# Optimization experiments

Measured on AMD Instinct MI355X. Metric: run time of the kernel, lower is better.

## Reference

```python
import jax, jax.numpy as jnp
import numpy as np

B, T, D, H = 4, 2048, 1024, 16
DK = D // H

def setup_inputs() -> dict:
    key = jax.random.key(0)
    k1, k2, k3 = jax.random.split(key, 3)
    s = 1.0 / np.sqrt(D)
    return {
        "x": jax.random.normal(k1, (B, T, D), dtype=jnp.float32),
        "W_qkv": jax.random.normal(k2, (D, 3 * D), dtype=jnp.float32) * s,
        "b_qkv": jnp.zeros((3 * D,), dtype=jnp.float32),
        "W_out": jax.random.normal(k3, (D, D), dtype=jnp.float32) * s,
        "b_out": jnp.zeros((D,), dtype=jnp.float32),
    }

def reference(x, W_qkv, b_qkv, W_out, b_out):
    Bx, Tx, C = x.shape
    qkv = x @ W_qkv + b_qkv                       # [B,T,3D]
    q, k, v = jnp.split(qkv, 3, axis=-1)
    # [B,T,D] -> [B,H,T,dk]
    def heads(t):
        return t.reshape(Bx, Tx, H, DK).transpose(0, 2, 1, 3)
    q, k, v = heads(q), heads(k), heads(v)
    scores = jnp.einsum('bhqd,bhkd->bhqk', q, k) / jnp.sqrt(jnp.float32(DK))
    causal = jnp.tril(jnp.ones((Tx, Tx), dtype=bool))  # [T,T]
    scores = jnp.where(causal[None, None], scores, -jnp.inf)
    attn = jax.nn.softmax(scores, axis=-1)        # dropout p=0 (eval)
    out = jnp.einsum('bhqk,bhkd->bhqd', attn, v)  # [B,H,T,dk]
    out = out.transpose(0, 2, 1, 3).reshape(Bx, Tx, C)
    return out @ W_out + b_out
```

## Files before the change

kernel.cpp:

```cpp
#include <hip/hip_runtime.h>
#include <hip/hip_bf16.h>
#include <stdint.h>

#define T_SEQ 2048
#define DMODEL 1024
#define NH 16
#define DKH 64
#define M_TOK 8192
#define N_QKV 3072
#define K_DIM 1024

#define ATTN_SC (0.125f * 1.44269504f)

typedef __attribute__((ext_vector_type(8))) short short8;
typedef __attribute__((ext_vector_type(4))) short short4v;
typedef __attribute__((ext_vector_type(4))) float float4v;
typedef __attribute__((ext_vector_type(2))) unsigned int uint2v;

__device__ inline short bf16_bits(float f) {
  __hip_bfloat16 h = __float2bfloat16(f);
  short s;
  __builtin_memcpy(&s, &h, 2);
  return s;
}

__device__ inline short4v pack4_bf16_fast(float a, float b, float c, float d) {
  unsigned ua = __builtin_bit_cast(unsigned, a) + 0x8000u;
  unsigned ub = __builtin_bit_cast(unsigned, b) + 0x8000u;
  unsigned uc = __builtin_bit_cast(unsigned, c) + 0x8000u;
  unsigned ud = __builtin_bit_cast(unsigned, d) + 0x8000u;
  uint2v uu = {(ua >> 16) | (ub & 0xFFFF0000u),
               (uc >> 16) | (ud & 0xFFFF0000u)};
  return __builtin_bit_cast(short4v, uu);
}

__device__ inline void async_load16(const void* g, void* l) {
  __builtin_amdgcn_global_load_lds(
      (const __attribute__((address_space(1))) unsigned int*)g,
      (__attribute__((address_space(3))) unsigned int*)l,
      16, 0, 0);
}


__global__ __launch_bounds__(256) void cvt_kernel(const float* __restrict__ in,
                                                  short* __restrict__ out, int n) {
  int idx = (blockIdx.x * 256 + threadIdx.x) * 4;
  if (idx < n) {
    float4v v = *(const float4v*)(in + idx);
    short4v o;
    o[0] = bf16_bits(v[0]); o[1] = bf16_bits(v[1]);
    o[2] = bf16_bits(v[2]); o[3] = bf16_bits(v[3]);
    *(short4v*)(out + idx) = o;
  }
}

__global__ __launch_bounds__(256) void transpose_cvt(const float* __restrict__ in,
                                                     short* __restrict__ out,
                                                     int K, int N) {
  __shared__ float tile[32][33];
  int n0 = blockIdx.x * 32, k0 = blockIdx.y * 32;
  int tx = threadIdx.x, ty = threadIdx.y;
  #pragma unroll
  for (int r = ty; r < 32; r += 8)
    tile[r][tx] = in[(size_t)(k0 + r) * N + n0 + tx];
  __syncthreads();
  #pragma unroll
  for (int r = ty; r < 32; r += 8)
    out[(size_t)(n0 + r) * K + k0 + tx] = bf16_bits(tile[tx][r]);
}


template <int MODE>
__global__ __launch_bounds__(256) void gemm_bt(
    const short* __restrict__ A, const short* __restrict__ Bt,
    const float* __restrict__ bias,
    short* __restrict__ Qb, short* __restrict__ Kf, short* __restrict__ Vf,
    float* __restrict__ Cout, int M, int N, int K) {
  __shared__ __align__(16) short As[128 * 32];
  __shared__ __align__(16) short Bs[128 * 32];
  const int tid = threadIdx.x;
  const int lane = tid & 63;
  const int wave = tid >> 6;
  const int m0 = blockIdx.y * 128;
  const int n0 = blockIdx.x * 128;
  const int wm = (wave >> 1) * 64;
  const int wn = (wave & 1) * 64;
  const int quad = lane >> 4;
  const int l16 = lane & 15;

  float4v acc[4][4] = {};

  const int r0 = tid >> 2,        o0 = (tid & 3) * 8;
  const int r1 = (tid + 256) >> 2, o1 = ((tid + 256) & 3) * 8;
  short* ldsA0 = As + (size_t)(wave * 64) * 8;
  short* ldsA1 = As + (size_t)(256 + wave * 64) * 8;
  short* ldsB0 = Bs + (size_t)(wave * 64) * 8;
  short* ldsB1 = Bs + (size_t)(256 + wave * 64) * 8;

  for (int kt = 0; kt < K; kt += 32) {
    async_load16(A  + (size_t)(m0 + r0) * K + kt + o0, ldsA0);
    async_load16(A  + (size_t)(m0 + r1) * K + kt + o1, ldsA1);
    async_load16(Bt + (size_t)(n0 + r0) * K + kt + o0, ldsB0);
    async_load16(Bt + (size_t)(n0 + r1) * K + kt + o1, ldsB1);
    __builtin_amdgcn_s_waitcnt(0);
    __syncthreads();

    short8 af[4], bfr[4];
    #pragma unroll
    for (int t = 0; t < 4; ++t)
      af[t] = *(const short8*)(As + (size_t)(wm + t * 16 + l16) * 32 + quad * 8);
    #pragma unroll
    for (int t = 0; t < 4; ++t)
      bfr[t] = *(const short8*)(Bs + (size_t)(wn + t * 16 + l16) * 32 + quad * 8);
    #pragma unroll
    for (int i = 0; i < 4; ++i)
      #pragma unroll
      for (int j = 0; j < 4; ++j)
        acc[i][j] = __builtin_amdgcn_mfma_f32_16x16x32_bf16(af[i], bfr[j], acc[i][j], 0, 0, 0);
    __syncthreads();
  }

  if (MODE == 0) {
    #pragma unroll
    for (int tj = 0; tj < 4; ++tj) {
      int col = n0 + wn + tj * 16 + l16;
      float bz = bias[col];
      int which = col >> 10;
      int d = col & 1023;
      int h = d >> 6, dk = d & 63;
      #pragma unroll
      for (int ti = 0; ti < 4; ++ti) {
        int rbase = m0 + wm + ti * 16 + quad * 4;
        int b = rbase >> 11;
        int t = rbase & 2047;
        size_t bhoff = (size_t)(b * NH + h) * (T_SEQ * DKH);
        if (which == 2) {
          short4v pv;
          #pragma unroll
          for (int i = 0; i < 4; ++i) pv[i] = bf16_bits(acc[ti][tj][i] + bz);
          size_t off = bhoff + (size_t)(t >> 6) * 4096 +
                       ((((t >> 4) & 3) * 4 + (dk >> 4)) * 4 + ((t >> 2) & 3)) * 64 +
                       (dk & 15) * 4;
          *(short4v*)(Vf + off) = pv;
        } else if (which == 0) {
          #pragma unroll
          for (int i = 0; i < 4; ++i)
            Qb[bhoff + (size_t)(t + i) * DKH + dk] =
                bf16_bits((acc[ti][tj][i] + bz) * ATTN_SC);
        } else {
          int h2 = dk >> 5, qd = (dk >> 3) & 3, w = dk & 7;
          size_t kbase = bhoff + (size_t)(t >> 6) * 4096 +
                         ((((t >> 4) & 3) * 2 + h2) * 4 + qd) * 128 + w;
          int lb = t & 15;
          #pragma unroll
          for (int i = 0; i < 4; ++i)
            Kf[kbase + (lb + i) * 8] = bf16_bits(acc[ti][tj][i] + bz);
        }
      }
    }
  } else {
    #pragma unroll
    for (int tj = 0; tj < 4; ++tj) {
      int col = n0 + wn + tj * 16 + l16;
      float bz = bias[col];
      #pragma unroll
      for (int ti = 0; ti < 4; ++ti)
        #pragma unroll
        for (int i = 0; i < 4; ++i) {
          int row = m0 + wm + ti * 16 + quad * 4 + i;
          Cout[(size_t)row * N + col] = acc[ti][tj][i] + bz;
        }
    }
  }
}


template <int MASK>
__device__ __forceinline__ void attn_tile(
    const short* __restrict__ Ks, const short* __restrict__ Vs,
    const short8 aq[2][2], short4v ones,
    float4v oc[2][4], float4v lc[2],
    int dkq, int quad, int l16) {
  const int mb = dkq + quad * 4 - l16;
  #pragma unroll
  for (int c = 0; c < 4; ++c) {
    short8 b0 = *(const short8*)(Ks + (c * 2 + 0) * 512 + quad * 128 + l16 * 8);
    short8 b1 = *(const short8*)(Ks + (c * 2 + 1) * 512 + quad * 128 + l16 * 8);
    short4v vf[4];
    #pragma unroll
    for (int d = 0; d < 4; ++d)
      vf[d] = *(const short4v*)(Vs + (c * 4 + d) * 256 + quad * 64 + l16 * 4);
    #pragma unroll
    for (int qi = 0; qi < 2; ++qi) {
      float4v z = {0.f, 0.f, 0.f, 0.f};
      z = __builtin_amdgcn_mfma_f32_16x16x32_bf16(b0, aq[qi][0], z, 0, 0, 0);
      z = __builtin_amdgcn_mfma_f32_16x16x32_bf16(b1, aq[qi][1], z, 0, 0, 0);
      float p[4];
      #pragma unroll
      for (int i = 0; i < 4; ++i) {
        p[i] = __builtin_amdgcn_exp2f(z[i]);
        if (MASK && (mb + c * 16 + i - qi * 16 > 0)) p[i] = 0.f;
      }
      short4v pb = pack4_bf16_fast(p[0], p[1], p[2], p[3]);
      lc[qi] = __builtin_amdgcn_mfma_f32_16x16x16bf16_1k(ones, pb, lc[qi], 0, 0, 0);
      #pragma unroll
      for (int d = 0; d < 4; ++d)
        oc[qi][d] = __builtin_amdgcn_mfma_f32_16x16x16bf16_1k(vf[d], pb, oc[qi][d], 0, 0, 0);
    }
  }
}

__global__ __launch_bounds__(256) void attn_kernel(const short* __restrict__ Qb,
                                                   const short* __restrict__ Kf,
                                                   const short* __restrict__ Vf,
                                                   short* __restrict__ Ao) {
  __shared__ __align__(16) short KsB[2][4096];
  __shared__ __align__(16) short VsB[2][4096];
  const int bh = blockIdx.x;
  const int qb = 15 - blockIdx.y;
  const int tid = threadIdx.x;
  const int lane = tid & 63, wave = tid >> 6;
  const int quad = lane >> 4, l16 = lane & 15;
  const int qw0 = qb * 128 + wave * 32;
  const int nkb = 2 * qb + 2;

  const short* Qg = Qb + ((size_t)bh * T_SEQ + qw0) * DKH;
  const short* Kg0 = Kf + (size_t)bh * (T_SEQ * DKH);
  const short* Vg0 = Vf + (size_t)bh * (T_SEQ * DKH);

  short8 aq[2][2];
  #pragma unroll
  for (int qi = 0; qi < 2; ++qi)
    #pragma unroll
    for (int h = 0; h < 2; ++h)
      aq[qi][h] = *(const short8*)(Qg + (size_t)(qi * 16 + l16) * DKH + h * 32 + quad * 8);

  float4v oc[2][4] = {};
  float4v lc[2] = {};
  short4v ones = {0x3F80, 0x3F80, 0x3F80, 0x3F80};

  async_load16(Kg0 + tid * 8,        &KsB[0][0] + wave * 512);
  async_load16(Kg0 + 2048 + tid * 8, &KsB[0][0] + 2048 + wave * 512);
  async_load16(Vg0 + tid * 8,        &VsB[0][0] + wave * 512);
  async_load16(Vg0 + 2048 + tid * 8, &VsB[0][0] + 2048 + wave * 512);

  for (int kb = 0; kb < nkb; ++kb) {
    __builtin_amdgcn_s_waitcnt(0);
    __syncthreads();

    if (kb + 1 < nkb) {
      const int nb = (kb + 1) & 1;
      const short* Kg = Kg0 + (size_t)(kb + 1) * 4096;
      const short* Vg = Vg0 + (size_t)(kb + 1) * 4096;
      async_load16(Kg + tid * 8,        &KsB[nb][0] + wave * 512);
      async_load16(Kg + 2048 + tid * 8, &KsB[nb][0] + 2048 + wave * 512);
      async_load16(Vg + tid * 8,        &VsB[nb][0] + wave * 512);
      async_load16(Vg + 2048 + tid * 8, &VsB[nb][0] + 2048 + wave * 512);
    }

    const int dkq = kb * 64 - qw0;
    if (dkq + 63 <= 0) {
      attn_tile<0>(&KsB[kb & 1][0], &VsB[kb & 1][0], aq, ones, oc, lc, dkq, quad, l16);
    } else if (dkq <= 31) {
      attn_tile<1>(&KsB[kb & 1][0], &VsB[kb & 1][0], aq, ones, oc, lc, dkq, quad, l16);
    }
  }

  const int b = bh >> 4, h = bh & 15;
  #pragma unroll
  for (int qi = 0; qi < 2; ++qi) {
    float rl = 1.0f / lc[qi][0];
    #pragma unroll
    for (int d = 0; d < 4; ++d) {
      short4v o;
      #pragma unroll
      for (int i = 0; i < 4; ++i) o[i] = bf16_bits(oc[qi][d][i] * rl);
      int t = qw0 + qi * 16 + l16;
      *(short4v*)(Ao + (size_t)(b * T_SEQ + t) * DMODEL + h * DKH + d * 16 + quad * 4) = o;
    }
  }
}


extern "C" void kernel_launch(void* const* d_in, const int* in_sizes, int n_in,
                              void* d_out, int out_size, void* d_ws, size_t ws_size,
                              hipStream_t stream) {
  const float* x    = (const float*)d_in[0];
  const float* Wqkv = (const float*)d_in[1];
  const float* bqkv = (const float*)d_in[2];
  const float* Wout = (const float*)d_in[3];
  const float* bout = (const float*)d_in[4];
  float* out = (float*)d_out;

  char* ws = (char*)d_ws;
  short* Xb    = (short*)(ws);
  short* Wqkvt = (short*)(ws + (16ull << 20));
  short* Woutt = (short*)(ws + (22ull << 20));
  short* Qb    = (short*)(ws + (24ull << 20));
  short* Kf    = (short*)(ws + (40ull << 20));
  short* Vf    = (short*)(ws + (56ull << 20));
  short* Ao    = (short*)(ws + (72ull << 20));

  cvt_kernel<<<(M_TOK * K_DIM / 4 + 255) / 256, 256, 0, stream>>>(x, Xb, M_TOK * K_DIM);
  dim3 tb(32, 8);
  transpose_cvt<<<dim3(N_QKV / 32, K_DIM / 32), tb, 0, stream>>>(Wqkv, Wqkvt, K_DIM, N_QKV);
  transpose_cvt<<<dim3(DMODEL / 32, K_DIM / 32), tb, 0, stream>>>(Wout, Woutt, K_DIM, DMODEL);

  gemm_bt<0><<<dim3(N_QKV / 128, M_TOK / 128), 256, 0, stream>>>(
      Xb, Wqkvt, bqkv, Qb, Kf, Vf, nullptr, M_TOK, N_QKV, K_DIM);

  attn_kernel<<<dim3(64, T_SEQ / 128), 256, 0, stream>>>(Qb, Kf, Vf, Ao);

  gemm_bt<1><<<dim3(DMODEL / 128, M_TOK / 128), 256, 0, stream>>>(
      Ao, Woutt, bout, nullptr, nullptr, nullptr, out, M_TOK, DMODEL, K_DIM);
}
```

Baseline: 273.0 us.

## Double-buffer GEMM LDS tiles and swap grid axes for block ordering

The GEMM kernel now keeps two LDS buffers and issues the async global-to-LDS loads for the next K tile right after the barrier, so they run while the MFMAs consume the current tile. This replaces the load-wait-compute-sync pattern and drops one barrier per iteration. The grid is also transposed so consecutive blocks walk along M for a fixed N column block, which changes L2 reuse of the weight and activation tiles. LDS use doubles, which may lower occupancy.

```diff
diff --git a/kernel.cpp b/kernel.cpp
--- a/kernel.cpp
+++ b/kernel.cpp
@@ -76,13 +76,13 @@
     const float* __restrict__ bias,
     short* __restrict__ Qb, short* __restrict__ Kf, short* __restrict__ Vf,
     float* __restrict__ Cout, int M, int N, int K) {
-  __shared__ __align__(16) short As[128 * 32];
-  __shared__ __align__(16) short Bs[128 * 32];
+  __shared__ __align__(16) short AsB[2][128 * 32];
+  __shared__ __align__(16) short BsB[2][128 * 32];
   const int tid = threadIdx.x;
   const int lane = tid & 63;
   const int wave = tid >> 6;
-  const int m0 = blockIdx.y * 128;
-  const int n0 = blockIdx.x * 128;
+  const int m0 = blockIdx.x * 128;
+  const int n0 = blockIdx.y * 128;
   const int wm = (wave >> 1) * 64;
   const int wn = (wave & 1) * 64;
   const int quad = lane >> 4;
@@ -92,19 +92,35 @@
 
   const int r0 = tid >> 2,        o0 = (tid & 3) * 8;
   const int r1 = (tid + 256) >> 2, o1 = ((tid + 256) & 3) * 8;
-  short* ldsA0 = As + (size_t)(wave * 64) * 8;
-  short* ldsA1 = As + (size_t)(256 + wave * 64) * 8;
-  short* ldsB0 = Bs + (size_t)(wave * 64) * 8;
-  short* ldsB1 = Bs + (size_t)(256 + wave * 64) * 8;
-
-  for (int kt = 0; kt < K; kt += 32) {
-    async_load16(A  + (size_t)(m0 + r0) * K + kt + o0, ldsA0);
-    async_load16(A  + (size_t)(m0 + r1) * K + kt + o1, ldsA1);
-    async_load16(Bt + (size_t)(n0 + r0) * K + kt + o0, ldsB0);
-    async_load16(Bt + (size_t)(n0 + r1) * K + kt + o1, ldsB1);
+  const int lo0 = wave * 512;
+  const int lo1 = 2048 + wave * 512;
+
+  const short* Ag0 = A  + (size_t)(m0 + r0) * K + o0;
+  const short* Ag1 = A  + (size_t)(m0 + r1) * K + o1;
+  const short* Bg0 = Bt + (size_t)(n0 + r0) * K + o0;
+  const short* Bg1 = Bt + (size_t)(n0 + r1) * K + o1;
+
+  async_load16(Ag0, &AsB[0][0] + lo0);
+  async_load16(Ag1, &AsB[0][0] + lo1);
+  async_load16(Bg0, &BsB[0][0] + lo0);
+  async_load16(Bg1, &BsB[0][0] + lo1);
+
+  const int nkt = K >> 5;
+  for (int it = 0; it < nkt; ++it) {
     __builtin_amdgcn_s_waitcnt(0);
     __syncthreads();
 
+    if (it + 1 < nkt) {
+      const int kt = (it + 1) << 5;
+      const int nb = (it + 1) & 1;
+      async_load16(Ag0 + kt, &AsB[nb][0] + lo0);
+      async_load16(Ag1 + kt, &AsB[nb][0] + lo1);
+      async_load16(Bg0 + kt, &BsB[nb][0] + lo0);
+      async_load16(Bg1 + kt, &BsB[nb][0] + lo1);
+    }
+
+    const short* As = &AsB[it & 1][0];
+    const short* Bs = &BsB[it & 1][0];
     short8 af[4], bfr[4];
     #pragma unroll
     for (int t = 0; t < 4; ++t)
@@ -117,7 +133,6 @@
       #pragma unroll
       for (int j = 0; j < 4; ++j)
         acc[i][j] = __builtin_amdgcn_mfma_f32_16x16x32_bf16(af[i], bfr[j], acc[i][j], 0, 0, 0);
-    __syncthreads();
   }
 
   if (MODE == 0) {
@@ -306,11 +321,11 @@
   transpose_cvt<<<dim3(N_QKV / 32, K_DIM / 32), tb, 0, stream>>>(Wqkv, Wqkvt, K_DIM, N_QKV);
   transpose_cvt<<<dim3(DMODEL / 32, K_DIM / 32), tb, 0, stream>>>(Wout, Woutt, K_DIM, DMODEL);
 
-  gemm_bt<0><<<dim3(N_QKV / 128, M_TOK / 128), 256, 0, stream>>>(
+  gemm_bt<0><<<dim3(M_TOK / 128, N_QKV / 128), 256, 0, stream>>>(
       Xb, Wqkvt, bqkv, Qb, Kf, Vf, nullptr, M_TOK, N_QKV, K_DIM);
 
   attn_kernel<<<dim3(64, T_SEQ / 128), 256, 0, stream>>>(Qb, Kf, Vf, Ao);
 
-  gemm_bt<1><<<dim3(DMODEL / 128, M_TOK / 128), 256, 0, stream>>>(
+  gemm_bt<1><<<dim3(M_TOK / 128, DMODEL / 128), 256, 0, stream>>>(
       Ao, Woutt, bout, nullptr, nullptr, nullptr, out, M_TOK, DMODEL, K_DIM);
 }
```

New measurement: 257.9 us. 5.5% less time.
